# Performance work log

Measured on AMD Instinct MI355X. Metric: run time of the kernel, lower is better.

Reference implementation:

```python
import jax, jax.numpy as jnp
import numpy as np

R = 4  # search_radius


def conv3(x, w, b):
    # 3x3 conv, padding=1 (SAME), NCHW / OIHW
    y = jax.lax.conv_general_dilated(x, w, window_strides=(1, 1), padding='SAME',
                                     dimension_numbers=('NCHW', 'OIHW', 'NCHW'))
    return y + b[None, :, None, None]


def bilinear_border(img, x, y):
    # torch F.grid_sample(mode='bilinear', padding_mode='border', align_corners=True)
    # img: (B,C,H,W); x,y: (B,H,W) unnormalized pixel coords
    B, C, H, W = img.shape
    x = jnp.clip(x, 0.0, W - 1.0)
    y = jnp.clip(y, 0.0, H - 1.0)
    x0 = jnp.floor(x)
    y0 = jnp.floor(y)
    x0i = x0.astype(jnp.int32)
    y0i = y0.astype(jnp.int32)
    x1i = jnp.minimum(x0i + 1, W - 1)
    y1i = jnp.minimum(y0i + 1, H - 1)
    wx = (x - x0)[..., None]
    wy = (y - y0)[..., None]
    imgt = jnp.transpose(img, (0, 2, 3, 1))  # (B,H,W,C)
    b = jnp.arange(B)[:, None, None]
    v00 = imgt[b, y0i, x0i]
    v01 = imgt[b, y0i, x1i]
    v10 = imgt[b, y1i, x0i]
    v11 = imgt[b, y1i, x1i]
    out = (v00 * (1 - wx) + v01 * wx) * (1 - wy) + (v10 * (1 - wx) + v11 * wx) * wy
    return jnp.transpose(out, (0, 3, 1, 2))


def _forward(feat1, feat2, initial_flow,
             fW1, fb1, fW2, fb2, fW3, fb3,
             rW1, rb1, rW2, rb2, rW3, rb3, rW4, rb4):
    relu = jax.nn.relu

    def extract(x):
        x = relu(conv3(x, fW1, fb1))
        x = relu(conv3(x, fW2, fb2))
        return relu(conv3(x, fW3, fb3))  # (B, 32, H, W)

    f1 = extract(feat1)
    f2 = extract(feat2)
    B, C, H, W = f1.shape
    yy, xx = jnp.meshgrid(jnp.arange(H, dtype=jnp.float32),
                          jnp.arange(W, dtype=jnp.float32), indexing='ij')
    # warp feat2 by initial flow; align_corners=True normalization cancels -> pixel coords + flow
    f2w = bilinear_border(f2, xx[None] + initial_flow[:, 0], yy[None] + initial_flow[:, 1])
    # search offsets, same order as search_grid.view(2,-1).t(): (dx, dy) row-major over (dy rows)
    coords = jnp.arange(-R, R + 1, dtype=jnp.float32)
    gy, gx = jnp.meshgrid(coords, coords, indexing='ij')
    offs = jnp.stack([gx.reshape(-1), gy.reshape(-1)], axis=1)  # (81, 2)
    xb = jnp.broadcast_to(xx[None], (B, H, W))
    yb = jnp.broadcast_to(yy[None], (B, H, W))

    def cost_fn(off):
        shifted = bilinear_border(f2w, xb + off[0], yb + off[1])
        return jnp.sum(f1 * shifted, axis=1)  # (B,H,W)

    cv = jnp.transpose(jax.lax.map(cost_fn, offs), (1, 0, 2, 3))  # (B,81,H,W)
    h = jnp.concatenate([cv, initial_flow], axis=1)  # (B,83,H,W)
    h = relu(conv3(h, rW1, rb1))
    h = relu(conv3(h, rW2, rb2))
    h = relu(conv3(h, rW3, rb3))
    return initial_flow + conv3(h, rW4, rb4)


def setup_inputs():
    key = jax.random.key(0)
    ks = jax.random.split(key, 12)
    B, H, W = 2, 256, 448
    FC = 64
    CV = (2 * R + 1) ** 2  # 81
    s = 0.05
    d = {}
    d['feat1'] = jax.random.normal(ks[0], (B, 3, H, W), jnp.float32)
    d['feat2'] = jax.random.normal(ks[1], (B, 3, H, W), jnp.float32)
    d['initial_flow'] = jax.random.normal(ks[2], (B, 2, H, W), jnp.float32)
    d['fW1'] = jax.random.normal(ks[3], (FC, 3, 3, 3), jnp.float32) * s
    d['fb1'] = jnp.zeros((FC,), jnp.float32)
    d['fW2'] = jax.random.normal(ks[4], (FC, FC, 3, 3), jnp.float32) * s
    d['fb2'] = jnp.zeros((FC,), jnp.float32)
    d['fW3'] = jax.random.normal(ks[5], (FC // 2, FC, 3, 3), jnp.float32) * s
    d['fb3'] = jnp.zeros((FC // 2,), jnp.float32)
    d['rW1'] = jax.random.normal(ks[6], (128, CV + 2, 3, 3), jnp.float32) * s
    d['rb1'] = jnp.zeros((128,), jnp.float32)
    d['rW2'] = jax.random.normal(ks[7], (128, 128, 3, 3), jnp.float32) * s
    d['rb2'] = jnp.zeros((128,), jnp.float32)
    d['rW3'] = jax.random.normal(ks[8], (64, 128, 3, 3), jnp.float32) * s
    d['rb3'] = jnp.zeros((64,), jnp.float32)
    d['rW4'] = jax.random.normal(ks[9], (2, 64, 3, 3), jnp.float32) * s
    d['rb4'] = jnp.zeros((2,), jnp.float32)
    return d


def reference(feat1, feat2, initial_flow,
              fW1, fb1, fW2, fb2, fW3, fb3,
              rW1, rb1, rW2, rb2, rW3, rb3, rW4, rb4):
    return _forward(feat1, feat2, initial_flow,
                    fW1, fb1, fW2, fb2, fW3, fb3,
                    rW1, rb1, rW2, rb2, rW3, rb3, rW4, rb4)
```

## Files before the change

### kernel.cpp

```cpp
#include <hip/hip_runtime.h>

#define HH 256
#define WW 448
#define HW (HH * WW)

typedef short bf16x8 __attribute__((ext_vector_type(8)));
typedef float f32x4 __attribute__((ext_vector_type(4)));
typedef unsigned int uint32;
typedef unsigned short ushort;

__device__ __forceinline__ ushort f2bf(float f) {
    uint32 u = __float_as_uint(f);
    u += 0x7fffu + ((u >> 16) & 1u);
    return (ushort)(u >> 16);
}

__device__ __forceinline__ void pack_one(
    int i, const float* __restrict__ w, ushort* __restrict__ wp,
    int CinReal, int CinPad, int Cout)
{
    int total = 9 * CinPad * Cout;
    if (i >= total) return;
    int ci = i & 31;
    int rest = i >> 5;
    int n = rest % Cout;
    int rest2 = rest / Cout;
    int KC = CinPad / 32;
    int kc = rest2 % KC;
    int tap = rest2 / KC;
    int cin = kc * 32 + ci;
    float v = (cin < CinReal) ? w[((size_t)n * CinReal + cin) * 9 + tap] : 0.f;
    wp[i] = f2bf(v);
}

__global__ __launch_bounds__(256) void pack_all_k(
    const float* fW2, const float* fW3, const float* rW1,
    const float* rW2, const float* rW3,
    ushort* wp2, ushort* wp3, ushort* wpr1, ushort* wpr2, ushort* wpr3)
{
    int i = blockIdx.x * 256 + threadIdx.x;
    pack_one(i, fW2, wp2, 64, 64, 64);
    pack_one(i, fW3, wp3, 64, 64, 32);
    pack_one(i, rW1, wpr1, 83, 96, 128);
    pack_one(i, rW2, wpr2, 128, 128, 128);
    pack_one(i, rW3, wpr3, 128, 128, 64);
}

template <int CIN, int COUT, int RELU>
__global__ __launch_bounds__(256, 4) void convmfma_k(
    const ushort* __restrict__ in, const ushort* __restrict__ wp,
    const float* __restrict__ bias, ushort* __restrict__ out,
    long inStride, long outStride)
{
    constexpr int KC = CIN / 32;
    constexpr int NPH = (CIN + 63) / 64;
    constexpr int CS = 72;
    constexpr int NG = (COUT >= 64) ? 4 : 2;
    constexpr int WN = (COUT / 16) / NG;
    constexpr int MG = 4 / NG;
    constexpr int WM = 8 / MG;

    __shared__ __align__(16) ushort lds[180 * CS];

    const int tid = threadIdx.x;
    const int x0 = blockIdx.x * 16;
    const int y0 = blockIdx.y * 8;
    in += (size_t)blockIdx.z * inStride;
    out += (size_t)blockIdx.z * outStride;

    const int wv = tid >> 6;
    const int lane = tid & 63;
    const int m = lane & 15;
    const int quad = lane >> 4;
    const int mbase = (wv % MG) * WM;
    const int nbase = (wv / MG) * WN * 16;

    const ushort* ldsA = lds + (mbase * 18 + m) * CS + quad * 8;
    const ushort* wpB = wp + ((size_t)nbase + m) * 32 + quad * 8;

    f32x4 acc[WM][WN];
#pragma unroll
    for (int t = 0; t < WM; ++t)
#pragma unroll
        for (int u = 0; u < WN; ++u)
            acc[t][u] = (f32x4){0.f, 0.f, 0.f, 0.f};

#pragma unroll 1
    for (int ph = 0; ph < NPH; ++ph) {
        const int C = (CIN - ph * 64 >= 64) ? 64 : (CIN - ph * 64);
        const int sh = (C == 64) ? 3 : 2;
        const int ch8 = C >> 3;

        if (ph) __syncthreads();
        for (int i = tid; i < 180 * ch8; i += 256) {
            int p = i >> sh, c8 = i & (ch8 - 1);
            int ry = p / 18, rx = p - ry * 18;
            int gy = y0 + ry - 1, gx = x0 + rx - 1;
            float4 v = make_float4(0.f, 0.f, 0.f, 0.f);
            if (gy >= 0 && gy < HH && gx >= 0 && gx < WW)
                v = *(const float4*)(in + ((size_t)gy * WW + gx) * CIN + ph * 64 + c8 * 8);
            *(float4*)(lds + p * CS + c8 * 8) = v;
        }
        __syncthreads();

        const int KCc = C / 32;
        const ushort* wpP = wpB + (size_t)(ph * 2) * COUT * 32;
#pragma unroll 1
        for (int tap = 0; tap < 9; ++tap) {
            const int ky = tap / 3;
            const int kx = tap - 3 * ky;
            const ushort* wpT = wpP + (size_t)tap * KC * COUT * 32;
#pragma unroll
            for (int kc = 0; kc < 2; ++kc) {
                if (kc >= KCc) break;
                bf16x8 b[WN];
#pragma unroll
                for (int u = 0; u < WN; ++u)
                    b[u] = *(const bf16x8*)(wpT + ((size_t)kc * COUT + u * 16) * 32);
#pragma unroll
                for (int th = 0; th < WM / 4; ++th) {
                    bf16x8 a[4];
#pragma unroll
                    for (int t4 = 0; t4 < 4; ++t4)
                        a[t4] = *(const bf16x8*)(ldsA +
                                ((th * 4 + t4 + ky) * 18 + kx) * CS + kc * 32);
#pragma unroll
                    for (int t4 = 0; t4 < 4; ++t4)
#pragma unroll
                        for (int u = 0; u < WN; ++u)
                            acc[th * 4 + t4][u] =
                                __builtin_amdgcn_mfma_f32_16x16x32_bf16(
                                    a[t4], b[u], acc[th * 4 + t4][u], 0, 0, 0);
                }
            }
        }
    }

#pragma unroll
    for (int u = 0; u < WN; ++u) {
        const int n = nbase + u * 16 + m;
        const float bs = bias[n];
#pragma unroll
        for (int t = 0; t < WM; ++t) {
            const int y = y0 + mbase + t;
#pragma unroll
            for (int r = 0; r < 4; ++r) {
                const int x = x0 + quad * 4 + r;
                float v = acc[t][u][r] + bs;
                if (RELU) v = fmaxf(v, 0.f);
                out[((size_t)y * WW + x) * COUT + n] = f2bf(v);
            }
        }
    }
}

__global__ __launch_bounds__(256) void fconv1_k(
    const float* __restrict__ in, const float* __restrict__ w,
    const float* __restrict__ bias, ushort* __restrict__ out,
    long inStride, long outStride)
{
    __shared__ float wl[1728];
    __shared__ float patch[3][4][18];
    const int tid = threadIdx.x;
    const int x0 = blockIdx.x * 16, y0 = blockIdx.y * 2;
    in += (size_t)blockIdx.z * inStride;
    out += (size_t)blockIdx.z * outStride;
    for (int i = tid; i < 1728; i += 256) wl[i] = w[i];
    for (int i = tid; i < 216; i += 256) {
        int ci = i / 72;
        int r = (i - ci * 72) / 18;
        int c = i - ci * 72 - r * 18;
        int gy = y0 + r - 1, gx = x0 + c - 1;
        patch[ci][r][c] = (gy >= 0 && gy < HH && gx >= 0 && gx < WW)
                              ? in[(size_t)ci * HW + gy * WW + gx] : 0.f;
    }
    __syncthreads();
    const int g = tid & 7;
    const int p = tid >> 3;
    const int py = p >> 4, px = p & 15;
    float acc[8];
#pragma unroll
    for (int j = 0; j < 8; ++j) acc[j] = bias[g * 8 + j];
#pragma unroll
    for (int ci = 0; ci < 3; ++ci)
#pragma unroll
        for (int k = 0; k < 9; ++k) {
            const int ky = k / 3, kx = k - 3 * ky;
            const float v = patch[ci][py + ky][px + kx];
#pragma unroll
            for (int j = 0; j < 8; ++j)
                acc[j] = fmaf(v, wl[(g * 8 + j) * 27 + ci * 9 + k], acc[j]);
        }
    ushort ov[8];
#pragma unroll
    for (int j = 0; j < 8; ++j) ov[j] = f2bf(fmaxf(acc[j], 0.f));
    const int y = y0 + py, x = x0 + px;
    *(float4*)(out + ((size_t)y * WW + x) * 64 + g * 8) = *(const float4*)ov;
}

__global__ __launch_bounds__(256) void warp_k(
    const ushort* __restrict__ f2, const float* __restrict__ flow,
    ushort* __restrict__ outp, long fStride, long flowStride, long oStride)
{
    int idx = blockIdx.x * 256 + threadIdx.x;
    if (idx >= HW) return;
    f2 += (size_t)blockIdx.y * fStride;
    flow += (size_t)blockIdx.y * flowStride;
    outp += (size_t)blockIdx.y * oStride;
    int y = idx / WW, x = idx - y * WW;
    float px_ = (float)x + flow[idx];
    float py_ = (float)y + flow[idx + HW];
    px_ = fminf(fmaxf(px_, 0.f), (float)(WW - 1));
    py_ = fminf(fmaxf(py_, 0.f), (float)(HH - 1));
    float fx0 = floorf(px_), fy0 = floorf(py_);
    int xi0 = (int)fx0, yi0 = (int)fy0;
    int xi1 = min(xi0 + 1, WW - 1), yi1 = min(yi0 + 1, HH - 1);
    float wx = px_ - fx0, wy = py_ - fy0;
    float w00 = (1.f - wx) * (1.f - wy), w01 = wx * (1.f - wy);
    float w10 = (1.f - wx) * wy, w11 = wx * wy;

    const uint32* a = (const uint32*)(f2 + ((size_t)yi0 * WW + xi0) * 32);
    const uint32* b = (const uint32*)(f2 + ((size_t)yi0 * WW + xi1) * 32);
    const uint32* c = (const uint32*)(f2 + ((size_t)yi1 * WW + xi0) * 32);
    const uint32* d = (const uint32*)(f2 + ((size_t)yi1 * WW + xi1) * 32);
    uint32 ov[16];
#pragma unroll
    for (int i = 0; i < 16; ++i) {
        uint32 wa = a[i], wb = b[i], wc = c[i], wd = d[i];
        float lo = __uint_as_float(wa << 16) * w00 + __uint_as_float(wb << 16) * w01 +
                   __uint_as_float(wc << 16) * w10 + __uint_as_float(wd << 16) * w11;
        float hi = __uint_as_float(wa & 0xffff0000u) * w00 + __uint_as_float(wb & 0xffff0000u) * w01 +
                   __uint_as_float(wc & 0xffff0000u) * w10 + __uint_as_float(wd & 0xffff0000u) * w11;
        ov[i] = ((uint32)f2bf(hi) << 16) | f2bf(lo);
    }
    uint32* o = (uint32*)(outp + (size_t)idx * 32);
#pragma unroll
    for (int i = 0; i < 16; ++i) o[i] = ov[i];
}

__global__ __launch_bounds__(256) void cost_mfma_k(
    const ushort* __restrict__ f1, const ushort* __restrict__ f2w,
    const float* __restrict__ flow, ushort* __restrict__ hb,
    long aStride, long flowStride)
{
    const int tid = threadIdx.x;
    const int wv = tid >> 6;
    const int lane = tid & 63;
    const int c = lane & 15;
    const int quad = lane >> 4;
    const int x0 = blockIdx.x * 16;
    const int y = blockIdx.y * 4 + wv;
    f1 += (size_t)blockIdx.z * aStride;
    f2w += (size_t)blockIdx.z * aStride;
    hb += (size_t)blockIdx.z * aStride;
    flow += (size_t)blockIdx.z * flowStride;

    const bf16x8 a = *(const bf16x8*)(f1 + ((size_t)y * WW + x0 + c) * 32 + quad * 8);

    const int xc0 = min(max(x0 - 4 + c, 0), WW - 1);
    const int xc1 = min(max(x0 + 12 + c, 0), WW - 1);

    ushort* hrow = hb + ((size_t)y * WW + x0) * 96;

#pragma unroll 1
    for (int dyi = 0; dyi < 9; ++dyi) {
        const int ys = min(max(y + dyi - 4, 0), HH - 1);
        const bf16x8 b0 = *(const bf16x8*)(f2w + ((size_t)ys * WW + xc0) * 32 + quad * 8);
        const bf16x8 b1 = *(const bf16x8*)(f2w + ((size_t)ys * WW + xc1) * 32 + quad * 8);
        f32x4 s0 = __builtin_amdgcn_mfma_f32_16x16x32_bf16(
            a, b0, (f32x4){0.f, 0.f, 0.f, 0.f}, 0, 0, 0);
        f32x4 s1 = __builtin_amdgcn_mfma_f32_16x16x32_bf16(
            a, b1, (f32x4){0.f, 0.f, 0.f, 0.f}, 0, 0, 0);

        ushort* hq = hrow + dyi * 9;
#pragma unroll
        for (int r = 0; r < 4; ++r) {
            const int m = quad * 4 + r;
            const int d0 = c - m;
            const int d1 = c + 16 - m;
            if (d0 >= 0 && d0 <= 8) hq[(size_t)m * 96 + d0] = f2bf(s0[r]);
            if (d1 <= 8) hq[(size_t)m * 96 + d1] = f2bf(s1[r]);
        }
    }

    if (lane < 16) {
        const int px = y * WW + x0 + lane;
        ushort* hq = hb + (size_t)px * 96;
        hq[81] = f2bf(flow[px]);
        hq[82] = f2bf(flow[px + HW]);
#pragma unroll
        for (int ch = 83; ch < 96; ++ch) hq[ch] = 0;
    }
}

__global__ __launch_bounds__(256) void rconv4_k(
    const ushort* __restrict__ in, const float* __restrict__ w,
    const float* __restrict__ bias, const float* __restrict__ flow,
    float* __restrict__ out, long inStride, long ioStride)
{
    __shared__ float wl[1152];
    for (int i = threadIdx.x; i < 1152; i += 256) wl[i] = w[i];
    __syncthreads();
    in += (size_t)blockIdx.y * inStride;
    flow += (size_t)blockIdx.y * ioStride;
    out += (size_t)blockIdx.y * ioStride;
    int px = blockIdx.x * 256 + threadIdx.x;
    if (px >= HW) return;
    int y = px / WW, x = px - y * WW;
    float a0 = bias[0], a1 = bias[1];
    for (int ky = 0; ky < 3; ++ky) {
        int gy = y + ky - 1;
        if (gy < 0 || gy >= HH) continue;
        for (int kx = 0; kx < 3; ++kx) {
            int gx = x + kx - 1;
            if (gx < 0 || gx >= WW) continue;
            const uint32* p = (const uint32*)(in + ((size_t)gy * WW + gx) * 64);
            int tap = ky * 3 + kx;
#pragma unroll
            for (int i = 0; i < 32; ++i) {
                uint32 wv = p[i];
                float lo = __uint_as_float(wv << 16);
                float hi = __uint_as_float(wv & 0xffff0000u);
                a0 = fmaf(lo, wl[(2 * i) * 9 + tap], a0);
                a0 = fmaf(hi, wl[(2 * i + 1) * 9 + tap], a0);
                a1 = fmaf(lo, wl[576 + (2 * i) * 9 + tap], a1);
                a1 = fmaf(hi, wl[576 + (2 * i + 1) * 9 + tap], a1);
            }
        }
    }
    out[px] = flow[px] + a0;
    out[px + HW] = flow[px + HW] + a1;
}

extern "C" void kernel_launch(void* const* d_in, const int* in_sizes, int n_in,
                              void* d_out, int out_size, void* d_ws, size_t ws_size,
                              hipStream_t stream)
{
    (void)in_sizes; (void)n_in; (void)out_size;
    const float* feat1 = (const float*)d_in[0];
    const float* feat2 = (const float*)d_in[1];
    const float* iflow = (const float*)d_in[2];
    const float* fW1 = (const float*)d_in[3];  const float* fb1 = (const float*)d_in[4];
    const float* fW2 = (const float*)d_in[5];  const float* fb2 = (const float*)d_in[6];
    const float* fW3 = (const float*)d_in[7];  const float* fb3 = (const float*)d_in[8];
    const float* rW1 = (const float*)d_in[9];  const float* rb1 = (const float*)d_in[10];
    const float* rW2 = (const float*)d_in[11]; const float* rb2 = (const float*)d_in[12];
    const float* rW3 = (const float*)d_in[13]; const float* rb3 = (const float*)d_in[14];
    const float* rW4 = (const float*)d_in[15]; const float* rb4 = (const float*)d_in[16];
    float* out = (float*)d_out;

    const size_t P = (size_t)HW;
    const size_t WTOT = (size_t)9 * (64 * 64 + 64 * 32 + 96 * 128 + 128 * 128 + 128 * 64);
    const size_t ARENA = 320 * P;
    ushort* ws0 = (ushort*)d_ws;
    ushort* wp2  = ws0;
    ushort* wp3  = wp2 + 9 * 64 * 64;
    ushort* wpr1 = wp3 + 9 * 64 * 32;
    ushort* wpr2 = wpr1 + 9 * 96 * 128;
    ushort* wpr3 = wpr2 + 9 * 128 * 128;
    ushort* arena = ws0 + WTOT;

    const bool merged = ws_size >= (WTOT + 2 * ARENA) * sizeof(ushort);
    const int nb = merged ? 2 : 1;
    const int nloop = merged ? 1 : 2;
    const long aS = merged ? (long)ARENA : 0;
    const long s3 = merged ? (long)(3 * P) : 0;
    const long s2 = merged ? (long)(2 * P) : 0;

    ushort* X0  = arena;
    ushort* X1  = X0 + 64 * P;
    ushort* F1  = X1 + 64 * P;
    ushort* F2  = F1 + 32 * P;
    ushort* F2W = F2 + 32 * P;
    ushort* Hb  = F2W + 32 * P;
    ushort* R1  = X0;
    ushort* R2  = F2W;
    ushort* R3  = F1;

    const dim3 blk(256);
    pack_all_k<<<dim3((9 * 128 * 128 + 255) / 256), blk, 0, stream>>>(
        fW2, fW3, rW1, rW2, rW3, wp2, wp3, wpr1, wpr2, wpr3);

    const dim3 gConv(WW / 16, HH / 8, nb);
    const dim3 gF1(WW / 16, HH / 2, nb);
    const dim3 gCost(WW / 16, HH / 4, nb);
    const int gPix = (HW + 255) / 256;

    for (int lb = 0; lb < nloop; ++lb) {
        const float* f1in = feat1 + (size_t)lb * 3 * P;
        const float* f2in = feat2 + (size_t)lb * 3 * P;
        const float* flw  = iflow + (size_t)lb * 2 * P;
        float* outb = out + (size_t)lb * 2 * P;

        fconv1_k<<<gF1, blk, 0, stream>>>(f2in, fW1, fb1, X0, s3, aS);
        convmfma_k<64, 64, 1><<<gConv, blk, 0, stream>>>(X0, wp2, fb2, X1, aS, aS);
        convmfma_k<64, 32, 1><<<gConv, blk, 0, stream>>>(X1, wp3, fb3, F2, aS, aS);
        warp_k<<<dim3(gPix, nb), blk, 0, stream>>>(F2, flw, F2W, aS, s2, aS);

        fconv1_k<<<gF1, blk, 0, stream>>>(f1in, fW1, fb1, X0, s3, aS);
        convmfma_k<64, 64, 1><<<gConv, blk, 0, stream>>>(X0, wp2, fb2, X1, aS, aS);
        convmfma_k<64, 32, 1><<<gConv, blk, 0, stream>>>(X1, wp3, fb3, F1, aS, aS);

        cost_mfma_k<<<gCost, blk, 0, stream>>>(F1, F2W, flw, Hb, aS, s2);

        convmfma_k<96, 128, 1><<<gConv, blk, 0, stream>>>(Hb, wpr1, rb1, R1, aS, aS);
        convmfma_k<128, 128, 1><<<gConv, blk, 0, stream>>>(R1, wpr2, rb2, R2, aS, aS);
        convmfma_k<128, 64, 1><<<gConv, blk, 0, stream>>>(R2, wpr3, rb3, R3, aS, aS);
        rconv4_k<<<dim3(gPix, nb), blk, 0, stream>>>(R3, rW4, rb4, flw, outb, aS, s2);
    }
}
```

Baseline: 506.2 us.

## Batch both feature-extraction passes into single launches and retune COUT=64 wave split

The feature extractor for feat1 and feat2 is now run as one set of launches with grid z covering both images and both batches. This halves the number of fconv1/conv launches and doubles each grid, and the workspace is re-laid out with a new aliasing scheme to match. Separately, 64-output-channel convs now split waves 2x2 over M/N instead of 4 over N. The buffer aliasing (F2W/Hb over XA, R1 over XB) is new and must not overwrite live data.

```diff
diff --git a/kernel.cpp b/kernel.cpp
--- a/kernel.cpp
+++ b/kernel.cpp
@@ -55,7 +55,7 @@
     constexpr int KC = CIN / 32;
     constexpr int NPH = (CIN + 63) / 64;
     constexpr int CS = 72;
-    constexpr int NG = (COUT >= 64) ? 4 : 2;
+    constexpr int NG = (COUT >= 128) ? 4 : 2;
     constexpr int WN = (COUT / 16) / NG;
     constexpr int MG = 4 / NG;
     constexpr int WM = 8 / MG;
@@ -155,16 +155,17 @@
 }
 
 __global__ __launch_bounds__(256) void fconv1_k(
-    const float* __restrict__ in, const float* __restrict__ w,
-    const float* __restrict__ bias, ushort* __restrict__ out,
-    long inStride, long outStride)
+    const float* __restrict__ f1src, const float* __restrict__ f2src,
+    const float* __restrict__ w, const float* __restrict__ bias,
+    ushort* __restrict__ out, long inStride, long outStride)
 {
     __shared__ float wl[1728];
     __shared__ float patch[3][4][18];
     const int tid = threadIdx.x;
     const int x0 = blockIdx.x * 16, y0 = blockIdx.y * 2;
-    in += (size_t)blockIdx.z * inStride;
-    out += (size_t)blockIdx.z * outStride;
+    const int z = blockIdx.z;
+    const float* in = ((z & 1) ? f2src : f1src) + (size_t)(z >> 1) * inStride;
+    out += (size_t)z * outStride;
     for (int i = tid; i < 1728; i += 256) wl[i] = w[i];
     for (int i = tid; i < 216; i += 256) {
         int ci = i / 72;
@@ -241,7 +242,7 @@
 __global__ __launch_bounds__(256) void cost_mfma_k(
     const ushort* __restrict__ f1, const ushort* __restrict__ f2w,
     const float* __restrict__ flow, ushort* __restrict__ hb,
-    long aStride, long flowStride)
+    long f1S, long f2wS, long hbS, long flowS)
 {
     const int tid = threadIdx.x;
     const int wv = tid >> 6;
@@ -250,10 +251,10 @@
     const int quad = lane >> 4;
     const int x0 = blockIdx.x * 16;
     const int y = blockIdx.y * 4 + wv;
-    f1 += (size_t)blockIdx.z * aStride;
-    f2w += (size_t)blockIdx.z * aStride;
-    hb += (size_t)blockIdx.z * aStride;
-    flow += (size_t)blockIdx.z * flowStride;
+    f1 += (size_t)blockIdx.z * f1S;
+    f2w += (size_t)blockIdx.z * f2wS;
+    hb += (size_t)blockIdx.z * hbS;
+    flow += (size_t)blockIdx.z * flowS;
 
     const bf16x8 a = *(const bf16x8*)(f1 + ((size_t)y * WW + x0 + c) * 32 + quad * 8);
 
@@ -351,7 +352,6 @@
 
     const size_t P = (size_t)HW;
     const size_t WTOT = (size_t)9 * (64 * 64 + 64 * 32 + 96 * 128 + 128 * 128 + 128 * 64);
-    const size_t ARENA = 320 * P;
     ushort* ws0 = (ushort*)d_ws;
     ushort* wp2  = ws0;
     ushort* wp3  = wp2 + 9 * 64 * 64;
@@ -360,29 +360,26 @@
     ushort* wpr3 = wpr2 + 9 * 128 * 128;
     ushort* arena = ws0 + WTOT;
 
-    const bool merged = ws_size >= (WTOT + 2 * ARENA) * sizeof(ushort);
+    const bool merged = ws_size >= (WTOT + 640 * P) * sizeof(ushort);
     const int nb = merged ? 2 : 1;
     const int nloop = merged ? 1 : 2;
-    const long aS = merged ? (long)ARENA : 0;
-    const long s3 = merged ? (long)(3 * P) : 0;
-    const long s2 = merged ? (long)(2 * P) : 0;
-
-    ushort* X0  = arena;
-    ushort* X1  = X0 + 64 * P;
-    ushort* F1  = X1 + 64 * P;
-    ushort* F2  = F1 + 32 * P;
-    ushort* F2W = F2 + 32 * P;
-    ushort* Hb  = F2W + 32 * P;
-    ushort* R1  = X0;
-    ushort* R2  = F2W;
-    ushort* R3  = F1;
+
+    ushort* XA = arena;
+    ushort* XB = XA + (size_t)(nb * 128) * P;
+    ushort* F  = XB + (size_t)(nb * 128) * P;
+    ushort* F2W = XA;
+    ushort* Hb  = XA + (size_t)(nb * 32) * P;
+    ushort* R1  = XB;
+    ushort* R2  = XA;
+    ushort* R3  = F;
 
     const dim3 blk(256);
     pack_all_k<<<dim3((9 * 128 * 128 + 255) / 256), blk, 0, stream>>>(
         fW2, fW3, rW1, rW2, rW3, wp2, wp3, wpr1, wpr2, wpr3);
 
-    const dim3 gConv(WW / 16, HH / 8, nb);
-    const dim3 gF1(WW / 16, HH / 2, nb);
+    const dim3 gConvX(WW / 16, HH / 8, nb * 2);
+    const dim3 gConvB(WW / 16, HH / 8, nb);
+    const dim3 gF1(WW / 16, HH / 2, nb * 2);
     const dim3 gCost(WW / 16, HH / 4, nb);
     const int gPix = (HW + 255) / 256;
 
@@ -392,20 +389,19 @@
         const float* flw  = iflow + (size_t)lb * 2 * P;
         float* outb = out + (size_t)lb * 2 * P;
 
-        fconv1_k<<<gF1, blk, 0, stream>>>(f2in, fW1, fb1, X0, s3, aS);
-        convmfma_k<64, 64, 1><<<gConv, blk, 0, stream>>>(X0, wp2, fb2, X1, aS, aS);
-        convmfma_k<64, 32, 1><<<gConv, blk, 0, stream>>>(X1, wp3, fb3, F2, aS, aS);
-        warp_k<<<dim3(gPix, nb), blk, 0, stream>>>(F2, flw, F2W, aS, s2, aS);
-
-        fconv1_k<<<gF1, blk, 0, stream>>>(f1in, fW1, fb1, X0, s3, aS);
-        convmfma_k<64, 64, 1><<<gConv, blk, 0, stream>>>(X0, wp2, fb2, X1, aS, aS);
-        convmfma_k<64, 32, 1><<<gConv, blk, 0, stream>>>(X1, wp3, fb3, F1, aS, aS);
-
-        cost_mfma_k<<<gCost, blk, 0, stream>>>(F1, F2W, flw, Hb, aS, s2);
-
-        convmfma_k<96, 128, 1><<<gConv, blk, 0, stream>>>(Hb, wpr1, rb1, R1, aS, aS);
-        convmfma_k<128, 128, 1><<<gConv, blk, 0, stream>>>(R1, wpr2, rb2, R2, aS, aS);
-        convmfma_k<128, 64, 1><<<gConv, blk, 0, stream>>>(R2, wpr3, rb3, R3, aS, aS);
-        rconv4_k<<<dim3(gPix, nb), blk, 0, stream>>>(R3, rW4, rb4, flw, outb, aS, s2);
-    }
-}
+        fconv1_k<<<gF1, blk, 0, stream>>>(f1in, f2in, fW1, fb1, XA, 3 * (long)P, 64 * (long)P);
+        convmfma_k<64, 64, 1><<<gConvX, blk, 0, stream>>>(XA, wp2, fb2, XB, 64 * (long)P, 64 * (long)P);
+        convmfma_k<64, 32, 1><<<gConvX, blk, 0, stream>>>(XB, wp3, fb3, F, 64 * (long)P, 32 * (long)P);
+
+        warp_k<<<dim3(gPix, nb), blk, 0, stream>>>(F + 32 * P, flw, F2W,
+                                                   64 * (long)P, 2 * (long)P, 32 * (long)P);
+
+        cost_mfma_k<<<gCost, blk, 0, stream>>>(F, F2W, flw, Hb,
+                                               64 * (long)P, 32 * (long)P, 96 * (long)P, 2 * (long)P);
+
+        convmfma_k<96, 128, 1><<<gConvB, blk, 0, stream>>>(Hb, wpr1, rb1, R1, 96 * (long)P, 128 * (long)P);
+        convmfma_k<128, 128, 1><<<gConvB, blk, 0, stream>>>(R1, wpr2, rb2, R2, 128 * (long)P, 128 * (long)P);
+        convmfma_k<128, 64, 1><<<gConvB, blk, 0, stream>>>(R2, wpr3, rb3, R3, 128 * (long)P, 64 * (long)P);
+        rconv4_k<<<dim3(gPix, nb), blk, 0, stream>>>(R3, rW4, rb4, flw, outb, 64 * (long)P, 2 * (long)P);
+    }
+}
```

Result: faster. 488.0 us (-3.6%).
